# Performance work log

Hardware: AMD Instinct MI355X
Metric: run time of the kernel (lower is better)

The kernel has to match this reference:

```python
import jax, jax.numpy as jnp
import numpy as np

B, S, D, H = 2, 2048, 2048, 16
DH = D // H
NEG = -1000000000.0


def setup_inputs() -> dict:
    key = jax.random.key(0)
    ks = jax.random.split(key, 5)
    return {
        "query_vector": jax.random.normal(ks[0], (B, S, D), dtype=jnp.float32),
        "key_vector": jax.random.normal(ks[1], (B, S, D), dtype=jnp.float32),
        "value_vector": jax.random.normal(ks[2], (B, S, D), dtype=jnp.float32),
        "W_qkv": jax.random.normal(ks[3], (D, 3 * D), dtype=jnp.float32) * (1.0 / np.sqrt(D)),
        "b_qkv": jax.random.normal(ks[4], (3 * D,), dtype=jnp.float32) * 0.01,
    }


def reference(query_vector, key_vector, value_vector, W_qkv, b_qkv):
    # NOTE: original forward only consumes query_vector; key/value args unused.
    qkv = query_vector @ W_qkv + b_qkv                      # [B, S, 3D]
    q, k, v = jnp.split(qkv, 3, axis=-1)                    # each [B, S, D]
    # Faithful to original: plain reshape (NOT transpose) into heads.
    q = q.reshape(B, H, S, DH)
    k = k.reshape(B, H, S, DH)
    v = v.reshape(B, H, S, DH)
    scores = jnp.einsum("bhqd,bhkd->bhqk", q, k) / np.float32(np.sqrt(DH))
    # torch.triu_indices(offset=0): mask j >= i (diagonal included), SET to -1e9.
    idx = jnp.arange(S)
    causal = idx[None, :] >= idx[:, None]                   # [S, S], True where masked
    scores = jnp.where(causal, jnp.float32(NEG), scores)
    attn = jax.nn.softmax(scores, axis=-1)
    out = jnp.einsum("bhqk,bhkd->bhqd", attn, v)            # [B, H, S, DH]
    # dropout is identity in eval mode
    return out.reshape(B, S, D)
```

## Files before the change

kernel.cpp:

```cpp
#include <hip/hip_runtime.h>
#include <hip/hip_bf16.h>
#include <stdint.h>

typedef unsigned short u16;
typedef short short8 __attribute__((ext_vector_type(8)));
typedef short short4v __attribute__((ext_vector_type(4)));
typedef float f32x4 __attribute__((ext_vector_type(4)));

#define CSL (0.08838834764831845f * 1.4426950408889634f)
#define NEGR -1.0e13f


__device__ __forceinline__ u16 f2b(float f) {
  union { float f; unsigned int u; } c; c.f = f;
  unsigned int u = c.u;
  u += 0x7fffu + ((u >> 16) & 1u);
  return (u16)(u >> 16);
}
__device__ __forceinline__ float b2f(u16 h) {
  union { float f; unsigned int u; } c; c.u = ((unsigned int)h) << 16;
  return c.f;
}

__global__ __launch_bounds__(256) void k_cast_q(const float* __restrict__ in, u16* __restrict__ out) {
  size_t idx = ((size_t)blockIdx.x * 256 + threadIdx.x) * 8;
  float4 f0 = *(const float4*)(in + idx);
  float4 f1 = *(const float4*)(in + idx + 4);
  short8 o;
  o[0] = (short)f2b(f0.x); o[1] = (short)f2b(f0.y); o[2] = (short)f2b(f0.z); o[3] = (short)f2b(f0.w);
  o[4] = (short)f2b(f1.x); o[5] = (short)f2b(f1.y); o[6] = (short)f2b(f1.z); o[7] = (short)f2b(f1.w);
  *(short8*)(out + idx) = o;
}

__global__ __launch_bounds__(256) void k_cast_wt(const float* __restrict__ W, u16* __restrict__ Wt) {
  __shared__ u16 L[64 * 68];
  const int t = threadIdx.x;
  const int nb = blockIdx.x * 64;
  const int kb = blockIdx.y * 64;
#pragma unroll
  for (int it = 0; it < 4; ++it) {
    int idx = it * 1024 + t * 4;
    int r = idx >> 6, c = idx & 63;
    float4 f = *(const float4*)(W + (size_t)(kb + r) * 6144 + nb + c);
    L[r * 68 + c + 0] = f2b(f.x);
    L[r * 68 + c + 1] = f2b(f.y);
    L[r * 68 + c + 2] = f2b(f.z);
    L[r * 68 + c + 3] = f2b(f.w);
  }
  __syncthreads();
#pragma unroll
  for (int it = 0; it < 4; ++it) {
    int idx = it * 1024 + t * 4;
    int i = idx >> 6, j = idx & 63;
    short4v o;
#pragma unroll
    for (int e = 0; e < 4; ++e) o[e] = (short)L[(j + e) * 68 + i];
    *(short4v*)(Wt + (size_t)(nb + i) * 2048 + kb + j) = o;
  }
}

__global__ __launch_bounds__(512, 1) void k_gemm256(const u16* __restrict__ A,
                                                    const u16* __restrict__ Bt,
                                                    const float* __restrict__ bias,
                                                    u16* __restrict__ qb,
                                                    u16* __restrict__ kbuf,
                                                    u16* __restrict__ vbuf) {
  __shared__ u16 As[2][16384];
  __shared__ u16 Bs[2][12288];
  const int t = threadIdx.x;
  const int ln = t & 63, w = t >> 6;
  const int lr = ln & 15, lg = ln >> 4;
  const int wm = w >> 2, wn = w & 3;
  const int Lid = blockIdx.x;
  const int xcd = Lid & 7, l = Lid >> 3;
  const int mt = (xcd & 1) * 8 + (l & 7);
  const int nt = (xcd >> 1) * 8 + (l >> 3);
  const int mb = mt * 256, nb = nt * 192;
  const int cswz = (lr & 7) * 8;
  const int srow = w * 8 + (ln >> 3);
  const int scol = ((ln & 7) ^ (ln >> 3)) * 8;

  const u16* Abase = A + (size_t)mb * 2048;
  const u16* Bbase = Bt + (size_t)nb * 2048;

  f32x4 acc[8][3] = {};

#define STAGE_S1(kt_, buf_)                                                                        \
  do {                                                                                             \
    const u16* as_ = Abase + (size_t)srow * 2048 + (kt_) * 64 + scol;                              \
    const u16* bs_ = Bbase + (size_t)srow * 2048 + (kt_) * 64 + scol;                              \
    __builtin_amdgcn_global_load_lds(                                                              \
        (const __attribute__((address_space(1))) void*)(as_),                                      \
        (__attribute__((address_space(3))) void*)(&As[buf_][0 * 4096 + w * 512]), 16, 0, 0);       \
    __builtin_amdgcn_global_load_lds(                                                              \
        (const __attribute__((address_space(1))) void*)(as_ + (size_t)2 * 64 * 2048),              \
        (__attribute__((address_space(3))) void*)(&As[buf_][2 * 4096 + w * 512]), 16, 0, 0);       \
    _Pragma("unroll")                                                                              \
    for (int p = 0; p < 3; ++p)                                                                    \
      __builtin_amdgcn_global_load_lds(                                                            \
          (const __attribute__((address_space(1))) void*)(bs_ + (size_t)p * 64 * 2048),            \
          (__attribute__((address_space(3))) void*)(&Bs[buf_][p * 4096 + w * 512]), 16, 0, 0);     \
  } while (0)

#define STAGE_S2(kt_, buf_)                                                                        \
  do {                                                                                             \
    const u16* as_ = Abase + (size_t)srow * 2048 + (kt_) * 64 + scol;                              \
    __builtin_amdgcn_global_load_lds(                                                              \
        (const __attribute__((address_space(1))) void*)(as_ + (size_t)1 * 64 * 2048),              \
        (__attribute__((address_space(3))) void*)(&As[buf_][1 * 4096 + w * 512]), 16, 0, 0);       \
    __builtin_amdgcn_global_load_lds(                                                              \
        (const __attribute__((address_space(1))) void*)(as_ + (size_t)3 * 64 * 2048),              \
        (__attribute__((address_space(3))) void*)(&As[buf_][3 * 4096 + w * 512]), 16, 0, 0);       \
  } while (0)

  STAGE_S1(0, 0);
  STAGE_S2(0, 0);
  asm volatile("s_waitcnt vmcnt(0)" ::: "memory");
  __builtin_amdgcn_s_barrier();

  for (int kt = 0; kt < 32; ++kt) {
    const int cur = kt & 1;
    const int ktn = (kt + 1) & 31;
    const u16* At = &As[cur][0];
    const u16* Bl = &Bs[cur][0];
    short8 af[4][2], bf[3][2];

    asm volatile("s_waitcnt vmcnt(2)" ::: "memory");
    __builtin_amdgcn_s_barrier();
#pragma unroll
    for (int mi = 0; mi < 4; ++mi)
#pragma unroll
      for (int ks = 0; ks < 2; ++ks)
        af[mi][ks] = *(const short8*)(At + (wm * 128 + mi * 16 + lr) * 64 + ((ks * 32 + lg * 8) ^ cswz));
#pragma unroll
    for (int ni = 0; ni < 3; ++ni)
#pragma unroll
      for (int ks = 0; ks < 2; ++ks)
        bf[ni][ks] = *(const short8*)(Bl + (wn * 48 + ni * 16 + lr) * 64 + ((ks * 32 + lg * 8) ^ cswz));
    STAGE_S1(ktn, cur ^ 1);
    __builtin_amdgcn_s_barrier();
    __builtin_amdgcn_s_setprio(1);
#pragma unroll
    for (int mi = 0; mi < 4; ++mi)
#pragma unroll
      for (int ni = 0; ni < 3; ++ni)
#pragma unroll
        for (int ks = 0; ks < 2; ++ks)
          acc[mi][ni] = __builtin_amdgcn_mfma_f32_16x16x32_bf16(af[mi][ks], bf[ni][ks], acc[mi][ni], 0, 0, 0);
    __builtin_amdgcn_s_setprio(0);

    asm volatile("s_waitcnt vmcnt(5)" ::: "memory");
    __builtin_amdgcn_s_barrier();
#pragma unroll
    for (int mi = 0; mi < 4; ++mi)
#pragma unroll
      for (int ks = 0; ks < 2; ++ks)
        af[mi][ks] = *(const short8*)(At + (wm * 128 + 64 + mi * 16 + lr) * 64 + ((ks * 32 + lg * 8) ^ cswz));
    STAGE_S2(ktn, cur ^ 1);
    __builtin_amdgcn_s_barrier();
    __builtin_amdgcn_s_setprio(1);
#pragma unroll
    for (int mi = 0; mi < 4; ++mi)
#pragma unroll
      for (int ni = 0; ni < 3; ++ni)
#pragma unroll
        for (int ks = 0; ks < 2; ++ks)
          acc[4 + mi][ni] = __builtin_amdgcn_mfma_f32_16x16x32_bf16(af[mi][ks], bf[ni][ks], acc[4 + mi][ni], 0, 0, 0);
    __builtin_amdgcn_s_setprio(0);
  }
#undef STAGE_S1
#undef STAGE_S2
  asm volatile("s_waitcnt vmcnt(0)" ::: "memory");

#pragma unroll
  for (int ni = 0; ni < 3; ++ni) {
    int ncol = nb + wn * 48 + ni * 16 + lr;
    u16* dst = (ncol < 2048) ? qb : (ncol < 4096 ? kbuf : vbuf);
    int nmod = ncol & 2047;
    float bv = bias[ncol];
#pragma unroll
    for (int m = 0; m < 8; ++m) {
#pragma unroll
      for (int r = 0; r < 4; ++r) {
        int mrow = mb + wm * 128 + m * 16 + lg * 4 + r;
        dst[(size_t)mrow * 2048 + nmod] = f2b(acc[m][ni][r] + bv);
      }
    }
  }
}

__global__ __launch_bounds__(256) void k_vtrans(const u16* __restrict__ v, u16* __restrict__ vt,
                                                float* __restrict__ part) {
  __shared__ u16 L[128 * 136];
  __shared__ float Ls2[256];
  const int t = threadIdx.x;
  const int bh = blockIdx.y, sc = blockIdx.x;
  const size_t base = (size_t)bh * 262144;
#pragma unroll
  for (int it = 0; it < 8; ++it) {
    int chunk = it * 256 + t;
    int s = chunk >> 4, d8 = (chunk & 15) * 8;
    *(short8*)(L + s * 136 + d8) = *(const short8*)(v + base + (size_t)(sc * 128 + s) * 128 + d8);
  }
  __syncthreads();
#pragma unroll
  for (int it = 0; it < 8; ++it) {
    int chunk = it * 256 + t;
    int dh = chunk >> 4, s8 = (chunk & 15) * 8;
    short8 o;
#pragma unroll
    for (int e = 0; e < 8; ++e) o[e] = (short)L[(s8 + e) * 136 + dh];
    *(short8*)(vt + base + (size_t)dh * 2048 + sc * 128 + s8) = o;
  }
  {
    const int dh = t & 127, seg = t >> 7;
    float ps = 0.f;
#pragma unroll 8
    for (int i = 0; i < 64; ++i) ps += b2f(L[(seg * 64 + i) * 136 + dh]);
    Ls2[t] = ps;
    __syncthreads();
    if (t < 128) part[((size_t)bh * 16 + sc) * 128 + t] = Ls2[t] + Ls2[t + 128];
  }
}

__global__ __launch_bounds__(256, 3) void k_attn(const u16* __restrict__ qb,
                                                 const u16* __restrict__ kb,
                                                 const u16* __restrict__ vt,
                                                 const float* __restrict__ part,
                                                 float* __restrict__ out) {
  __shared__ u16 Ks[64 * 136];
  __shared__ u16 Vs[128 * 72];
  __shared__ u16 Ps[4][16 * 72];
  const int t = threadIdx.x;
  const int ln = t & 63, wv = t >> 6;
  const int lr = ln & 15, lg = ln >> 4;
  const int L = blockIdx.y * 32 + blockIdx.x;
  const int wl = (L & 7) * 128 + (L >> 3);
  const int bh = wl >> 5;
  const int qt = 31 - (wl & 31);
  const size_t base = (size_t)bh * 262144;
  const u16* Qh = qb + base;
  const u16* Kh = kb + base;
  const u16* Vth = vt + base;
  float* Oh = out + base;
  const int qs = qt * 64;

  short8 qf[4];
  {
    int qr = qs + wv * 16 + lr;
#pragma unroll
    for (int ks = 0; ks < 4; ++ks)
      qf[ks] = *(const short8*)(Qh + (size_t)qr * 128 + ks * 32 + lg * 8);
  }
  float lsum[4] = {0.f, 0.f, 0.f, 0.f};
  f32x4 acc[8];
  const f32x4 fz = {0.f, 0.f, 0.f, 0.f};
#pragma unroll
  for (int oj = 0; oj < 8; ++oj) acc[oj] = fz;

  u16* Pw = &Ps[wv][0];
  const int nkt = qt + 1;
  for (int kt = 0; kt < nkt; ++kt) {
#pragma unroll
    for (int it = 0; it < 4; ++it) {
      int chunk = it * 256 + t;
      int sk = chunk >> 4, d8 = (chunk & 15) * 8;
      *(short8*)(Ks + sk * 136 + d8) = *(const short8*)(Kh + (size_t)(kt * 64 + sk) * 128 + d8);
    }
#pragma unroll
    for (int it = 0; it < 4; ++it) {
      int chunk = it * 256 + t;
      int dh = chunk >> 3, s8 = (chunk & 7) * 8;
      *(short8*)(Vs + dh * 72 + s8) = *(const short8*)(Vth + (size_t)dh * 2048 + kt * 64 + s8);
    }
    __syncthreads();

    f32x4 s[4];
#pragma unroll
    for (int ni = 0; ni < 4; ++ni) s[ni] = fz;
#pragma unroll
    for (int ks = 0; ks < 4; ++ks) {
#pragma unroll
      for (int ni = 0; ni < 4; ++ni) {
        short8 kf = *(const short8*)(Ks + (ni * 16 + lr) * 136 + ks * 32 + lg * 8);
        s[ni] = __builtin_amdgcn_mfma_f32_16x16x32_bf16(qf[ks], kf, s[ni], 0, 0, 0);
      }
    }
    if (kt == qt) {
#pragma unroll
      for (int ni = 0; ni < 4; ++ni) {
        int col = kt * 64 + ni * 16 + lr;
#pragma unroll
        for (int r = 0; r < 4; ++r) {
          int row = qs + wv * 16 + lg * 4 + r;
          if (col >= row) s[ni][r] = NEGR;
        }
      }
    }
#pragma unroll
    for (int ni = 0; ni < 4; ++ni)
#pragma unroll
      for (int r = 0; r < 4; ++r) {
        u16 h = f2b(exp2f(s[ni][r] * CSL));
        Pw[(lg * 4 + r) * 72 + ni * 16 + lr] = h;
        lsum[r] += b2f(h);
      }
#pragma unroll
    for (int ks2 = 0; ks2 < 2; ++ks2) {
      short8 pa = *(const short8*)(Pw + lr * 72 + ks2 * 32 + lg * 8);
#pragma unroll
      for (int oj = 0; oj < 8; ++oj) {
        short8 vf = *(const short8*)(Vs + (oj * 16 + lr) * 72 + ks2 * 32 + lg * 8);
        acc[oj] = __builtin_amdgcn_mfma_f32_16x16x32_bf16(pa, vf, acc[oj], 0, 0, 0);
      }
    }
    __syncthreads();
  }

  float rl[4];
#pragma unroll
  for (int r = 0; r < 4; ++r) {
    float sa = lsum[r];
#pragma unroll
    for (int d = 1; d < 16; d <<= 1) sa += __shfl_xor(sa, d, 64);
    rl[r] = 1.0f / sa;
  }
#pragma unroll
  for (int oj = 0; oj < 8; ++oj)
#pragma unroll
    for (int r = 0; r < 4; ++r) {
      int row = qs + wv * 16 + lg * 4 + r;
      float val = acc[oj][r] * rl[r];
      if (qt == 0 && wv == 0 && lg == 0 && r == 0) {
        float vs = 0.f;
#pragma unroll
        for (int sc = 0; sc < 16; ++sc) vs += part[(size_t)bh * 2048 + sc * 128 + oj * 16 + lr];
        val = vs * (1.0f / 2048.0f);
      }
      Oh[(size_t)row * 128 + oj * 16 + lr] = val;
    }
}

extern "C" void kernel_launch(void* const* d_in, const int* in_sizes, int n_in,
                              void* d_out, int out_size, void* d_ws, size_t ws_size,
                              hipStream_t stream) {
  (void)in_sizes; (void)n_in; (void)out_size; (void)ws_size;
  const float* q_in = (const float*)d_in[0];
  const float* W = (const float*)d_in[3];
  const float* bias = (const float*)d_in[4];
  float* out = (float*)d_out;

  u16* qbf = (u16*)d_ws;
  u16* wtb = qbf + (size_t)4096 * 2048;
  u16* qb  = wtb + (size_t)6144 * 2048;
  u16* kbf = qb  + (size_t)4096 * 2048;
  u16* vbf = kbf + (size_t)4096 * 2048;
  u16* vt  = vbf + (size_t)4096 * 2048;
  float* part = (float*)(vt + (size_t)4096 * 2048);

  k_cast_q<<<4096, 256, 0, stream>>>(q_in, qbf);
  k_cast_wt<<<dim3(96, 32), 256, 0, stream>>>(W, wtb);
  k_gemm256<<<512, 512, 0, stream>>>(qbf, wtb, bias, qb, kbf, vbf);
  k_vtrans<<<dim3(16, 32), 256, 0, stream>>>(vbf, vt, part);
  k_attn<<<dim3(32, 32), 256, 0, stream>>>(qb, kbf, vt, part, out);
}
```

Before: 227.0 us.

## Split QKV GEMM main loop into four k-half phases with finer staged prefetch

Restructures the QKV projection GEMM loop from two phases into four. Each phase loads one k-half of the fragments, issues part of the next tile's global-to-LDS prefetch, and runs a smaller MFMA batch. The vmcnt waits shift so that the prefetch of the A and B pieces overlaps more finely with compute, and fewer fragment registers are live at once. In exchange there are more barriers per iteration, and the reworked vmcnt accounting must stay correct against the in-flight loads.

New measurement: 235.0 us. +3.5%, slower.

```diff
diff --git a/kernel.cpp b/kernel.cpp
--- a/kernel.cpp
+++ b/kernel.cpp
@@ -85,23 +85,25 @@
 
   f32x4 acc[8][3] = {};
 
-#define STAGE_S1(kt_, buf_)                                                                        \
+#define STAGE_S1A(kt_, buf_)                                                                       \
   do {                                                                                             \
     const u16* as_ = Abase + (size_t)srow * 2048 + (kt_) * 64 + scol;                              \
-    const u16* bs_ = Bbase + (size_t)srow * 2048 + (kt_) * 64 + scol;                              \
     __builtin_amdgcn_global_load_lds(                                                              \
         (const __attribute__((address_space(1))) void*)(as_),                                      \
         (__attribute__((address_space(3))) void*)(&As[buf_][0 * 4096 + w * 512]), 16, 0, 0);       \
     __builtin_amdgcn_global_load_lds(                                                              \
         (const __attribute__((address_space(1))) void*)(as_ + (size_t)2 * 64 * 2048),              \
         (__attribute__((address_space(3))) void*)(&As[buf_][2 * 4096 + w * 512]), 16, 0, 0);       \
+  } while (0)
+#define STAGE_S1B(kt_, buf_)                                                                       \
+  do {                                                                                             \
+    const u16* bs_ = Bbase + (size_t)srow * 2048 + (kt_) * 64 + scol;                              \
     _Pragma("unroll")                                                                              \
     for (int p = 0; p < 3; ++p)                                                                    \
       __builtin_amdgcn_global_load_lds(                                                            \
           (const __attribute__((address_space(1))) void*)(bs_ + (size_t)p * 64 * 2048),            \
           (__attribute__((address_space(3))) void*)(&Bs[buf_][p * 4096 + w * 512]), 16, 0, 0);     \
   } while (0)
-
 #define STAGE_S2(kt_, buf_)                                                                        \
   do {                                                                                             \
     const u16* as_ = Abase + (size_t)srow * 2048 + (kt_) * 64 + scol;                              \
@@ -113,9 +115,10 @@
         (__attribute__((address_space(3))) void*)(&As[buf_][3 * 4096 + w * 512]), 16, 0, 0);       \
   } while (0)
 
-  STAGE_S1(0, 0);
+  STAGE_S1A(0, 0);
+  STAGE_S1B(0, 0);
   STAGE_S2(0, 0);
-  asm volatile("s_waitcnt vmcnt(0)" ::: "memory");
+  asm volatile("s_waitcnt vmcnt(2)" ::: "memory");
   __builtin_amdgcn_s_barrier();
 
   for (int kt = 0; kt < 32; ++kt) {
@@ -123,52 +126,73 @@
     const int ktn = (kt + 1) & 31;
     const u16* At = &As[cur][0];
     const u16* Bl = &Bs[cur][0];
-    short8 af[4][2], bf[3][2];
-
+    short8 af0[4], af1[4], bf0[3], bf1[3];
+
+#pragma unroll
+    for (int mi = 0; mi < 4; ++mi)
+      af0[mi] = *(const short8*)(At + (wm * 128 + mi * 16 + lr) * 64 + ((lg * 8) ^ cswz));
+#pragma unroll
+    for (int ni = 0; ni < 3; ++ni)
+      bf0[ni] = *(const short8*)(Bl + (wn * 48 + ni * 16 + lr) * 64 + ((lg * 8) ^ cswz));
+    STAGE_S1A(ktn, cur ^ 1);
+    __builtin_amdgcn_s_barrier();
+    __builtin_amdgcn_s_setprio(1);
+#pragma unroll
+    for (int mi = 0; mi < 4; ++mi)
+#pragma unroll
+      for (int ni = 0; ni < 3; ++ni)
+        acc[mi][ni] = __builtin_amdgcn_mfma_f32_16x16x32_bf16(af0[mi], bf0[ni], acc[mi][ni], 0, 0, 0);
+    __builtin_amdgcn_s_setprio(0);
+    __builtin_amdgcn_s_barrier();
+
+#pragma unroll
+    for (int mi = 0; mi < 4; ++mi)
+      af1[mi] = *(const short8*)(At + (wm * 128 + mi * 16 + lr) * 64 + ((32 + lg * 8) ^ cswz));
+#pragma unroll
+    for (int ni = 0; ni < 3; ++ni)
+      bf1[ni] = *(const short8*)(Bl + (wn * 48 + ni * 16 + lr) * 64 + ((32 + lg * 8) ^ cswz));
+    STAGE_S1B(ktn, cur ^ 1);
+    __builtin_amdgcn_s_barrier();
+    __builtin_amdgcn_s_setprio(1);
+#pragma unroll
+    for (int mi = 0; mi < 4; ++mi)
+#pragma unroll
+      for (int ni = 0; ni < 3; ++ni)
+        acc[mi][ni] = __builtin_amdgcn_mfma_f32_16x16x32_bf16(af1[mi], bf1[ni], acc[mi][ni], 0, 0, 0);
+    __builtin_amdgcn_s_setprio(0);
+    asm volatile("s_waitcnt vmcnt(5)" ::: "memory");
+    __builtin_amdgcn_s_barrier();
+
+#pragma unroll
+    for (int mi = 0; mi < 4; ++mi)
+      af0[mi] = *(const short8*)(At + (wm * 128 + 64 + mi * 16 + lr) * 64 + ((lg * 8) ^ cswz));
+    STAGE_S2(ktn, cur ^ 1);
+    __builtin_amdgcn_s_barrier();
+    __builtin_amdgcn_s_setprio(1);
+#pragma unroll
+    for (int mi = 0; mi < 4; ++mi)
+#pragma unroll
+      for (int ni = 0; ni < 3; ++ni)
+        acc[4 + mi][ni] = __builtin_amdgcn_mfma_f32_16x16x32_bf16(af0[mi], bf0[ni], acc[4 + mi][ni], 0, 0, 0);
+    __builtin_amdgcn_s_setprio(0);
+    __builtin_amdgcn_s_barrier();
+
+#pragma unroll
+    for (int mi = 0; mi < 4; ++mi)
+      af1[mi] = *(const short8*)(At + (wm * 128 + 64 + mi * 16 + lr) * 64 + ((32 + lg * 8) ^ cswz));
+    __builtin_amdgcn_s_barrier();
+    __builtin_amdgcn_s_setprio(1);
+#pragma unroll
+    for (int mi = 0; mi < 4; ++mi)
+#pragma unroll
+      for (int ni = 0; ni < 3; ++ni)
+        acc[4 + mi][ni] = __builtin_amdgcn_mfma_f32_16x16x32_bf16(af1[mi], bf1[ni], acc[4 + mi][ni], 0, 0, 0);
+    __builtin_amdgcn_s_setprio(0);
     asm volatile("s_waitcnt vmcnt(2)" ::: "memory");
     __builtin_amdgcn_s_barrier();
-#pragma unroll
-    for (int mi = 0; mi < 4; ++mi)
-#pragma unroll
-      for (int ks = 0; ks < 2; ++ks)
-        af[mi][ks] = *(const short8*)(At + (wm * 128 + mi * 16 + lr) * 64 + ((ks * 32 + lg * 8) ^ cswz));
-#pragma unroll
-    for (int ni = 0; ni < 3; ++ni)
-#pragma unroll
-      for (int ks = 0; ks < 2; ++ks)
-        bf[ni][ks] = *(const short8*)(Bl + (wn * 48 + ni * 16 + lr) * 64 + ((ks * 32 + lg * 8) ^ cswz));
-    STAGE_S1(ktn, cur ^ 1);
-    __builtin_amdgcn_s_barrier();
-    __builtin_amdgcn_s_setprio(1);
-#pragma unroll
-    for (int mi = 0; mi < 4; ++mi)
-#pragma unroll
-      for (int ni = 0; ni < 3; ++ni)
-#pragma unroll
-        for (int ks = 0; ks < 2; ++ks)
-          acc[mi][ni] = __builtin_amdgcn_mfma_f32_16x16x32_bf16(af[mi][ks], bf[ni][ks], acc[mi][ni], 0, 0, 0);
-    __builtin_amdgcn_s_setprio(0);
-
-    asm volatile("s_waitcnt vmcnt(5)" ::: "memory");
-    __builtin_amdgcn_s_barrier();
-#pragma unroll
-    for (int mi = 0; mi < 4; ++mi)
-#pragma unroll
-      for (int ks = 0; ks < 2; ++ks)
-        af[mi][ks] = *(const short8*)(At + (wm * 128 + 64 + mi * 16 + lr) * 64 + ((ks * 32 + lg * 8) ^ cswz));
-    STAGE_S2(ktn, cur ^ 1);
-    __builtin_amdgcn_s_barrier();
-    __builtin_amdgcn_s_setprio(1);
-#pragma unroll
-    for (int mi = 0; mi < 4; ++mi)
-#pragma unroll
-      for (int ni = 0; ni < 3; ++ni)
-#pragma unroll
-        for (int ks = 0; ks < 2; ++ks)
-          acc[4 + mi][ni] = __builtin_amdgcn_mfma_f32_16x16x32_bf16(af[mi][ks], bf[ni][ks], acc[4 + mi][ni], 0, 0, 0);
-    __builtin_amdgcn_s_setprio(0);
-  }
-#undef STAGE_S1
+  }
+#undef STAGE_S1A
+#undef STAGE_S1B
 #undef STAGE_S2
   asm volatile("s_waitcnt vmcnt(0)" ::: "memory");
 
```
